# Performance work log

Hardware: AMD Instinct MI355X
Metric: run time of the kernel (lower is better)

The kernel has to match this reference:

```python
import jax, jax.numpy as jnp
import numpy as np

V, H, L, B, S = 32000, 1024, 2, 8, 256


def setup_inputs() -> dict:
    key = jax.random.key(0)
    ks = jax.random.split(key, 12)
    s = 1.0 / np.sqrt(H)  # PyTorch LSTM/Linear init range
    u = lambda k, shape: jax.random.uniform(k, shape, jnp.float32, -s, s)
    return {
        "x": jax.random.randint(ks[0], (B, S), 0, V, dtype=jnp.int32),
        "h0": jnp.zeros((L, B, H), jnp.float32),
        "c0": jnp.zeros((L, B, H), jnp.float32),
        "w_ih0": u(ks[1], (4 * H, V)),
        "w_hh0": u(ks[2], (4 * H, H)),
        "b_ih0": u(ks[3], (4 * H,)),
        "b_hh0": u(ks[4], (4 * H,)),
        "w_ih1": u(ks[5], (4 * H, H)),
        "w_hh1": u(ks[6], (4 * H, H)),
        "b_ih1": u(ks[7], (4 * H,)),
        "b_hh1": u(ks[8], (4 * H,)),
        "fc_w": u(ks[9], (V, H)),
        "fc_b": u(ks[10], (V,)),
    }


def _lstm_layer(xproj, h0, c0, w_hh):
    """xproj: [S,B,4H] input-to-gate projection (biases folded in).
    Gate order i,f,g,o matches PyTorch."""
    def step(carry, xp):
        h, c = carry
        g = xp + h @ w_hh.T  # [B,4H]
        i, f, gg, o = jnp.split(g, 4, axis=-1)
        c = jax.nn.sigmoid(f) * c + jax.nn.sigmoid(i) * jnp.tanh(gg)
        h = jax.nn.sigmoid(o) * jnp.tanh(c)
        return (h, c), h
    (hT, cT), hs = jax.lax.scan(step, (h0, c0), xproj)
    return hs, hT, cT


def reference(x, h0, c0, w_ih0, w_hh0, b_ih0, b_hh0, w_ih1, w_hh1, b_ih1, b_hh1, fc_w, fc_b):
    # F.one_hot(x, V).float() @ w_ih0.T  ==  gather of rows of w_ih0.T (identical math)
    xp0 = jnp.take(w_ih0.T, x, axis=0) + (b_ih0 + b_hh0)  # [B,S,4H]
    xp0 = xp0.transpose(1, 0, 2)  # [S,B,4H] for time-major scan
    h1s, h1T, c1T = _lstm_layer(xp0, h0[0], c0[0], w_hh0)
    xp1 = h1s @ w_ih1.T + (b_ih1 + b_hh1)  # [S,B,4H]
    h2s, h2T, c2T = _lstm_layer(xp1, h0[1], c0[1], w_hh1)
    out = h2s.transpose(1, 0, 2).reshape(-1, H)  # [B*S,H]
    logits = out @ fc_w.T + fc_b  # [B*S,V]
    hn = jnp.stack([h1T, h2T])
    cn = jnp.stack([c1T, c2T])
    return logits, (hn, cn)
```

## Files before the change

### kernel.cpp

```cpp
#include <hip/hip_runtime.h>
#include <cmath>

typedef float  f32x4  __attribute__((ext_vector_type(4)));
typedef float  f32x2  __attribute__((ext_vector_type(2)));
typedef __bf16 bf16x8 __attribute__((ext_vector_type(8)));

static constexpr int HN  = 1024;
static constexpr int VN  = 32000;
static constexpr int BN  = 8;
static constexpr int SN  = 256;
static constexpr int H4N = 4096;

__global__ __launch_bounds__(256) void k_gather(const int* __restrict__ x,
    const float* __restrict__ w_ih0, const float* __restrict__ b_ih0,
    const float* __restrict__ b_hh0, float* __restrict__ xp) {
  int bid = blockIdx.x;
  int t = bid >> 3, b = bid & 7;
  int tok = x[b * SN + t];
  const float* col = w_ih0 + tok;
  float* dst = xp + (size_t)bid * H4N;
  for (int r = threadIdx.x; r < H4N; r += 256)
    dst[r] = col[(size_t)r * VN] + b_ih0[r] + b_hh0[r];
}

__global__ __launch_bounds__(256, 1) void k_lstm(
    const float* __restrict__ xp,
    const float* __restrict__ w_hh,
    const float* __restrict__ h0,
    const float* __restrict__ c0,
    float* __restrict__ hs,
    float* __restrict__ hn, float* __restrict__ cn,
    unsigned* __restrict__ bar) {
  __shared__ float wL[16][1024];
  __shared__ float hL[8192];
  __shared__ float red[8][4][4][32];
  __shared__ float gates[16][8];
  __shared__ float cL[32];

  const int tid = threadIdx.x;
  const int wg  = blockIdx.x;
  const int u0  = wg * 4;

  for (int it = 0; it < 16; ++it) {
    int g = it >> 2, u = it & 3;
    int k4 = tid;
    int k4s = k4 ^ ((k4 >> 3) & 7);
    f32x4 v = *(const f32x4*)&w_hh[((size_t)g * HN + u0 + u) * HN + k4 * 4];
    *(f32x4*)&wL[it][k4s * 4] = v;
  }
  if (tid < 32) cL[tid] = c0[(tid & 7) * HN + u0 + (tid >> 3)];

  const int ks = tid & 31, rg = (tid >> 5) & 3, bg = tid >> 7;
  const int ksx = ks & 7;
  const int hb = tid & 7;
  const int hk = tid >> 3;

  const int prow = tid >> 3, pb = tid & 7;
  const int pg = prow >> 2, pu = prow & 3;
  const size_t pofs = (size_t)pb * H4N + (size_t)pg * HN + u0 + pu;

  for (int t = 0; t < SN; ++t) {
    float xpv = 0.f;
    if (tid < 128) xpv = xp[(size_t)t * (BN * H4N) + pofs];

    const float* hsrc = (t == 0) ? h0 : (hs + (size_t)(t - 1) * (BN * HN));
    const unsigned long long* hsrc8 =
        (const unsigned long long*)hsrc + (size_t)hb * 512 + hk;
    unsigned long long rv[16];
    #pragma unroll
    for (int j = 0; j < 16; ++j)
      rv[j] = __hip_atomic_load((unsigned long long*)(hsrc8 + j * 32),
                                __ATOMIC_RELAXED, __HIP_MEMORY_SCOPE_AGENT);
    #pragma unroll
    for (int j = 0; j < 16; ++j) {
      int k64 = hk + j * 32;
      int k4 = k64 >> 1, half = k64 & 1;
      int idx = ((k4 << 3) | hb) ^ ((k4 >> 3) & 7);
      *(f32x2*)&hL[idx * 4 + half * 2] = __builtin_bit_cast(f32x2, rv[j]);
    }
    __syncthreads();

    float acc[4][4] = {};
    #pragma unroll
    for (int j = 0; j < 8; ++j) {
      int k4 = ks * 8 + j;
      int k4s = k4 ^ ksx;
      f32x4 wv[4], hv[4];
      #pragma unroll
      for (int ri = 0; ri < 4; ++ri)
        wv[ri] = *(const f32x4*)&wL[rg * 4 + ri][k4s * 4];
      #pragma unroll
      for (int bi = 0; bi < 4; ++bi) {
        int idx = ((k4 << 3) | (bg * 4 + bi)) ^ ksx;
        hv[bi] = *(const f32x4*)&hL[idx * 4];
      }
      #pragma unroll
      for (int ri = 0; ri < 4; ++ri)
        #pragma unroll
        for (int bi = 0; bi < 4; ++bi)
          acc[ri][bi] += wv[ri][0]*hv[bi][0] + wv[ri][1]*hv[bi][1]
                       + wv[ri][2]*hv[bi][2] + wv[ri][3]*hv[bi][3];
    }
    #pragma unroll
    for (int ri = 0; ri < 4; ++ri)
      #pragma unroll
      for (int bi = 0; bi < 4; ++bi)
        red[rg * 2 + bg][ri][bi][ks] = acc[ri][bi];
    __syncthreads();

    if (tid < 128) {
      int rrg = prow >> 2, ri = prow & 3, bbg = pb >> 2, bi = pb & 3;
      const float* rp = red[rrg * 2 + bbg][ri][bi];
      float s = 0.f;
      #pragma unroll
      for (int q = 0; q < 32; ++q) s += rp[(q + tid) & 31];
      gates[prow][pb] = s + xpv;
    }
    __syncthreads();

    if (tid < 32) {
      int u = tid >> 3, b = tid & 7;
      float gi = gates[0 * 4 + u][b], gf = gates[1 * 4 + u][b];
      float gg = gates[2 * 4 + u][b], go = gates[3 * 4 + u][b];
      float si = 1.f / (1.f + expf(-gi));
      float sf = 1.f / (1.f + expf(-gf));
      float so = 1.f / (1.f + expf(-go));
      float c = sf * cL[tid] + si * tanhf(gg);
      float h = so * tanhf(c);
      cL[tid] = c;
      __hip_atomic_store(&hs[(size_t)t * (BN * HN) + b * HN + u0 + u], h,
                         __ATOMIC_RELAXED, __HIP_MEMORY_SCOPE_AGENT);
      if (t == SN - 1) {
        hn[b * HN + u0 + u] = h;
        cn[b * HN + u0 + u] = c;
      }
    }

    if (t != SN - 1) {
      if (tid == 0) {
        asm volatile("s_waitcnt vmcnt(0)" ::: "memory");
        __hip_atomic_fetch_add(&bar[(wg & 7) * 32], 1u,
                               __ATOMIC_RELAXED, __HIP_MEMORY_SCOPE_AGENT);
      }
      if (tid < 8) {
        unsigned tgt = 32u * (unsigned)(t + 1);
        while (__hip_atomic_load(&bar[tid * 32], __ATOMIC_RELAXED,
                                 __HIP_MEMORY_SCOPE_AGENT) < tgt)
          __builtin_amdgcn_s_sleep(1);
      }
      __syncthreads();
    } else {
      __syncthreads();
    }
  }
}

__global__ __launch_bounds__(256) void k_split(const float* __restrict__ src,
    __bf16* __restrict__ hi, __bf16* __restrict__ lo) {
  int i = (blockIdx.x * 256 + threadIdx.x) * 4;
  f32x4 v = *(const f32x4*)&src[i];
  #pragma unroll
  for (int j = 0; j < 4; ++j) {
    __bf16 h = (__bf16)v[j];
    hi[i + j] = h;
    lo[i + j] = (__bf16)(v[j] - (float)h);
  }
}

__global__ __launch_bounds__(256) void k_gemm(const __bf16* __restrict__ Ahi,
    const __bf16* __restrict__ Alo, const float* __restrict__ Bsrc,
    const float* __restrict__ bias1, const float* __restrict__ bias2,
    float* __restrict__ C, int Mt, int N, int permute) {
  __shared__ __bf16 sAh[128][32], sAl[128][32], sBh[128][32], sBl[128][32];
  int bid = blockIdx.x;
  int tn = bid / Mt, tm = bid % Mt;
  int tid = threadIdx.x, lane = tid & 63, wid = tid >> 6;
  int wr = wid >> 1, wc = wid & 1;
  f32x4 acc[4][4] = {};
  const size_t K = 1024;

  for (int kk = 0; kk < 1024; kk += 32) {
    __syncthreads();
    #pragma unroll
    for (int it = 0; it < 2; ++it) {
      int c = it * 256 + tid;
      int r = c >> 2, k8 = (c & 3) * 8;
      size_t ga = (size_t)(tm * 128 + r) * K + kk + k8;
      *(bf16x8*)&sAh[r][k8] = *(const bf16x8*)&Ahi[ga];
      *(bf16x8*)&sAl[r][k8] = *(const bf16x8*)&Alo[ga];
      size_t gb = (size_t)(tn * 128 + r) * K + kk + k8;
      f32x4 x0 = *(const f32x4*)&Bsrc[gb];
      f32x4 x1 = *(const f32x4*)&Bsrc[gb + 4];
      bf16x8 bh, bl;
      #pragma unroll
      for (int j = 0; j < 4; ++j) {
        __bf16 h0 = (__bf16)x0[j]; bh[j]     = h0; bl[j]     = (__bf16)(x0[j] - (float)h0);
        __bf16 h1 = (__bf16)x1[j]; bh[4 + j] = h1; bl[4 + j] = (__bf16)(x1[j] - (float)h1);
      }
      *(bf16x8*)&sBh[r][k8] = bh;
      *(bf16x8*)&sBl[r][k8] = bl;
    }
    __syncthreads();

    int kq = (lane >> 4) * 8;
    bf16x8 ah[4], al[4], bh[4], bl[4];
    #pragma unroll
    for (int i = 0; i < 4; ++i) {
      int ra = wr * 64 + i * 16 + (lane & 15);
      ah[i] = *(const bf16x8*)&sAh[ra][kq];
      al[i] = *(const bf16x8*)&sAl[ra][kq];
      int rb = wc * 64 + i * 16 + (lane & 15);
      bh[i] = *(const bf16x8*)&sBh[rb][kq];
      bl[i] = *(const bf16x8*)&sBl[rb][kq];
    }
    #pragma unroll
    for (int i = 0; i < 4; ++i)
      #pragma unroll
      for (int j = 0; j < 4; ++j) {
        acc[i][j] = __builtin_amdgcn_mfma_f32_16x16x32_bf16(ah[i], bh[j], acc[i][j], 0, 0, 0);
        acc[i][j] = __builtin_amdgcn_mfma_f32_16x16x32_bf16(ah[i], bl[j], acc[i][j], 0, 0, 0);
        acc[i][j] = __builtin_amdgcn_mfma_f32_16x16x32_bf16(al[i], bh[j], acc[i][j], 0, 0, 0);
      }
  }

  #pragma unroll
  for (int j = 0; j < 4; ++j) {
    int gcol = tn * 128 + wc * 64 + j * 16 + (lane & 15);
    float bv = bias1[gcol] + (bias2 ? bias2[gcol] : 0.f);
    #pragma unroll
    for (int i = 0; i < 4; ++i) {
      #pragma unroll
      for (int r = 0; r < 4; ++r) {
        int row = tm * 128 + wr * 64 + i * 16 + ((lane >> 4) << 2) + r;
        int orow = permute ? ((row & 7) * 256 + (row >> 3)) : row;
        C[(size_t)orow * N + gcol] = acc[i][j][r] + bv;
      }
    }
  }
}

extern "C" void kernel_launch(void* const* d_in, const int* in_sizes, int n_in,
                              void* d_out, int out_size, void* d_ws, size_t ws_size,
                              hipStream_t stream) {
  (void)in_sizes; (void)n_in; (void)out_size; (void)ws_size;
  const int*   x     = (const int*)  d_in[0];
  const float* h0    = (const float*)d_in[1];
  const float* c0    = (const float*)d_in[2];
  const float* w_ih0 = (const float*)d_in[3];
  const float* w_hh0 = (const float*)d_in[4];
  const float* b_ih0 = (const float*)d_in[5];
  const float* b_hh0 = (const float*)d_in[6];
  const float* w_ih1 = (const float*)d_in[7];
  const float* w_hh1 = (const float*)d_in[8];
  const float* b_ih1 = (const float*)d_in[9];
  const float* b_hh1 = (const float*)d_in[10];
  const float* fc_w  = (const float*)d_in[11];
  const float* fc_b  = (const float*)d_in[12];
  float* out = (float*)d_out;
  float* ws  = (float*)d_ws;

  float* xp   = ws;
  float* h1s  = ws + 8388608;
  float* h2s  = ws + 10485760;
  __bf16* Ahi = (__bf16*)(ws + 12582912);
  __bf16* Alo = (__bf16*)(ws + 13631488);
  unsigned* bar = (unsigned*)(ws + 14680064);

  const size_t LOG = (size_t)2048 * VN;
  float* hn = out + LOG;
  float* cn = out + LOG + 16384;

  hipMemsetAsync(bar, 0, 4096 * sizeof(unsigned), stream);

  k_gather<<<SN * BN, 256, 0, stream>>>(x, w_ih0, b_ih0, b_hh0, xp);

  k_lstm<<<256, 256, 0, stream>>>(xp, w_hh0, h0, c0, h1s, hn, cn, bar);

  k_split<<<2048, 256, 0, stream>>>(h1s, Ahi, Alo);
  k_gemm<<<16 * 32, 256, 0, stream>>>(Ahi, Alo, w_ih1, b_ih1, b_hh1, xp,
                                      16, H4N, 0);

  k_lstm<<<256, 256, 0, stream>>>(xp, w_hh1, h0 + BN * HN, c0 + BN * HN,
                                  h2s, hn + BN * HN, cn + BN * HN, bar + 2048);

  k_split<<<2048, 256, 0, stream>>>(h2s, Ahi, Alo);
  k_gemm<<<16 * 250, 256, 0, stream>>>(Ahi, Alo, fc_w, fc_b, nullptr, out,
                                       16, VN, 1);
}
```

Measured before the change: 4.546 ms.

## Use per-XCD leader blocks to relay hidden state through local buffers

Replaces the all-to-all grid barrier in the persistent LSTM kernel with a hierarchical scheme. One elected leader block per XCD polls the 64 per-group counters, reads the previous hidden state and copies it into a per-XCD double-buffered scratch area, then raises a flag. The other blocks on that XCD wait only on the flag and read the copy with sc0 loads, so that cross-die polling and coherent traffic are confined to one block per XCD. The cost is an extra serialized hop (leader copy, then flag) on the critical path every step, and correctness now depends on how blocks are placed across XCDs and on the memory ordering of the relaxed atomics.

```diff
diff --git a/kernel.cpp b/kernel.cpp
--- a/kernel.cpp
+++ b/kernel.cpp
@@ -30,16 +30,28 @@
     const float* __restrict__ c0,
     float* __restrict__ hs,
     float* __restrict__ hn, float* __restrict__ cn,
-    unsigned* __restrict__ bar) {
+    unsigned* __restrict__ bar,
+    unsigned* __restrict__ flag,
+    unsigned* __restrict__ elect,
+    float* __restrict__ xbuf) {
   __shared__ float wL[16][1024];
   __shared__ float hL[8192];
   __shared__ float red[8][4][4][32];
   __shared__ float gates[16][8];
   __shared__ float cL[32];
+  __shared__ unsigned meta[2];
 
   const int tid = threadIdx.x;
   const int wg  = blockIdx.x;
   const int u0  = wg * 4;
+
+  unsigned xcc;
+  asm volatile("s_getreg_b32 %0, hwreg(HW_REG_XCC_ID)" : "=s"(xcc));
+  if (tid == 0) {
+    meta[0] = xcc & 7;
+    meta[1] = __hip_atomic_fetch_add(&elect[(xcc & 7) * 32], 1u,
+                                     __ATOMIC_RELAXED, __HIP_MEMORY_SCOPE_AGENT);
+  }
 
   for (int it = 0; it < 16; ++it) {
     int g = it >> 2, u = it & 3;
@@ -49,6 +61,9 @@
     *(f32x4*)&wL[it][k4s * 4] = v;
   }
   if (tid < 32) cL[tid] = c0[(tid & 7) * HN + u0 + (tid >> 3)];
+  __syncthreads();
+  const int  myxcd  = (int)meta[0];
+  const bool leader = (meta[1] == 0u);
 
   const int ks = tid & 31, rg = (tid >> 5) & 3, bg = tid >> 7;
   const int ksx = ks & 7;
@@ -63,14 +78,73 @@
     float xpv = 0.f;
     if (tid < 128) xpv = xp[(size_t)t * (BN * H4N) + pofs];
 
-    const float* hsrc = (t == 0) ? h0 : (hs + (size_t)(t - 1) * (BN * HN));
-    const unsigned long long* hsrc8 =
-        (const unsigned long long*)hsrc + (size_t)hb * 512 + hk;
+    float* xbp = xbuf + ((size_t)(t & 1) * 8 + myxcd) * 8192;
     unsigned long long rv[16];
-    #pragma unroll
-    for (int j = 0; j < 16; ++j)
-      rv[j] = __hip_atomic_load((unsigned long long*)(hsrc8 + j * 32),
-                                __ATOMIC_RELAXED, __HIP_MEMORY_SCOPE_AGENT);
+    if (t == 0) {
+      const unsigned long long* s8 =
+          (const unsigned long long*)h0 + (size_t)hb * 512 + hk;
+      #pragma unroll
+      for (int j = 0; j < 16; ++j) rv[j] = s8[j * 32];
+    } else if (leader) {
+      if (tid < 64) {
+        unsigned tgt = 4u * (unsigned)t;
+        while (__hip_atomic_load(&bar[tid * 32], __ATOMIC_RELAXED,
+                                 __HIP_MEMORY_SCOPE_AGENT) < tgt)
+          __builtin_amdgcn_s_sleep(1);
+      }
+      __syncthreads();
+      const unsigned long long* hsrc8 =
+          (const unsigned long long*)(hs + (size_t)(t - 1) * (BN * HN))
+          + (size_t)hb * 512 + hk;
+      #pragma unroll
+      for (int j = 0; j < 16; ++j)
+        rv[j] = __hip_atomic_load((unsigned long long*)(hsrc8 + j * 32),
+                                  __ATOMIC_RELAXED, __HIP_MEMORY_SCOPE_AGENT);
+      unsigned long long* xb8 =
+          (unsigned long long*)xbp + (size_t)hb * 512 + hk;
+      #pragma unroll
+      for (int j = 0; j < 16; ++j) xb8[j * 32] = rv[j];
+    } else {
+      if (tid == 0) {
+        while (__hip_atomic_load(&flag[myxcd * 32], __ATOMIC_RELAXED,
+                                 __HIP_MEMORY_SCOPE_AGENT) < (unsigned)t)
+          __builtin_amdgcn_s_sleep(1);
+      }
+      __syncthreads();
+      const unsigned long long* xb8 =
+          (const unsigned long long*)xbp + (size_t)hb * 512 + hk;
+      unsigned long long a = (unsigned long long)xb8;
+      unsigned long long r0, r1, r2, r3, r4, r5, r6, r7;
+      unsigned long long r8, r9, r10, r11, r12, r13, r14, r15;
+      asm volatile(
+        "global_load_dwordx2 %0, %16, off sc0\n\t"
+        "global_load_dwordx2 %1, %16, off offset:256 sc0\n\t"
+        "global_load_dwordx2 %2, %16, off offset:512 sc0\n\t"
+        "global_load_dwordx2 %3, %16, off offset:768 sc0\n\t"
+        "global_load_dwordx2 %4, %16, off offset:1024 sc0\n\t"
+        "global_load_dwordx2 %5, %16, off offset:1280 sc0\n\t"
+        "global_load_dwordx2 %6, %16, off offset:1536 sc0\n\t"
+        "global_load_dwordx2 %7, %16, off offset:1792 sc0\n\t"
+        "global_load_dwordx2 %8, %16, off offset:2048 sc0\n\t"
+        "global_load_dwordx2 %9, %16, off offset:2304 sc0\n\t"
+        "global_load_dwordx2 %10, %16, off offset:2560 sc0\n\t"
+        "global_load_dwordx2 %11, %16, off offset:2816 sc0\n\t"
+        "global_load_dwordx2 %12, %16, off offset:3072 sc0\n\t"
+        "global_load_dwordx2 %13, %16, off offset:3328 sc0\n\t"
+        "global_load_dwordx2 %14, %16, off offset:3584 sc0\n\t"
+        "global_load_dwordx2 %15, %16, off offset:3840 sc0\n\t"
+        "s_waitcnt vmcnt(0)"
+        : "=&v"(r0), "=&v"(r1), "=&v"(r2), "=&v"(r3),
+          "=&v"(r4), "=&v"(r5), "=&v"(r6), "=&v"(r7),
+          "=&v"(r8), "=&v"(r9), "=&v"(r10), "=&v"(r11),
+          "=&v"(r12), "=&v"(r13), "=&v"(r14), "=&v"(r15)
+        : "v"(a) : "memory");
+      rv[0] = r0;  rv[1] = r1;  rv[2] = r2;  rv[3] = r3;
+      rv[4] = r4;  rv[5] = r5;  rv[6] = r6;  rv[7] = r7;
+      rv[8] = r8;  rv[9] = r9;  rv[10] = r10; rv[11] = r11;
+      rv[12] = r12; rv[13] = r13; rv[14] = r14; rv[15] = r15;
+    }
+
     #pragma unroll
     for (int j = 0; j < 16; ++j) {
       int k64 = hk + j * 32;
@@ -79,6 +153,9 @@
       *(f32x2*)&hL[idx * 4 + half * 2] = __builtin_bit_cast(f32x2, rv[j]);
     }
     __syncthreads();
+    if (t > 0 && leader && tid == 0)
+      __hip_atomic_fetch_add(&flag[myxcd * 32], 1u,
+                             __ATOMIC_RELAXED, __HIP_MEMORY_SCOPE_AGENT);
 
     float acc[4][4] = {};
     #pragma unroll
@@ -139,14 +216,8 @@
     if (t != SN - 1) {
       if (tid == 0) {
         asm volatile("s_waitcnt vmcnt(0)" ::: "memory");
-        __hip_atomic_fetch_add(&bar[(wg & 7) * 32], 1u,
+        __hip_atomic_fetch_add(&bar[(wg >> 2) * 32], 1u,
                                __ATOMIC_RELAXED, __HIP_MEMORY_SCOPE_AGENT);
-      }
-      if (tid < 8) {
-        unsigned tgt = 32u * (unsigned)(t + 1);
-        while (__hip_atomic_load(&bar[tid * 32], __ATOMIC_RELAXED,
-                                 __HIP_MEMORY_SCOPE_AGENT) < tgt)
-          __builtin_amdgcn_s_sleep(1);
       }
       __syncthreads();
     } else {
@@ -264,24 +335,34 @@
   float* h2s  = ws + 10485760;
   __bf16* Ahi = (__bf16*)(ws + 12582912);
   __bf16* Alo = (__bf16*)(ws + 13631488);
-  unsigned* bar = (unsigned*)(ws + 14680064);
+  unsigned* U = (unsigned*)(ws + 14680064);
+  unsigned* bar0   = U;
+  unsigned* bar1   = U + 2048;
+  unsigned* flag0  = U + 4096;
+  unsigned* flag1  = U + 4352;
+  unsigned* elect0 = U + 4608;
+  unsigned* elect1 = U + 4864;
+  float* xbuf0 = ws + 14688256;
+  float* xbuf1 = ws + 14819328;
 
   const size_t LOG = (size_t)2048 * VN;
   float* hn = out + LOG;
   float* cn = out + LOG + 16384;
 
-  hipMemsetAsync(bar, 0, 4096 * sizeof(unsigned), stream);
+  hipMemsetAsync(U, 0, 5120 * sizeof(unsigned), stream);
 
   k_gather<<<SN * BN, 256, 0, stream>>>(x, w_ih0, b_ih0, b_hh0, xp);
 
-  k_lstm<<<256, 256, 0, stream>>>(xp, w_hh0, h0, c0, h1s, hn, cn, bar);
+  k_lstm<<<256, 256, 0, stream>>>(xp, w_hh0, h0, c0, h1s, hn, cn,
+                                  bar0, flag0, elect0, xbuf0);
 
   k_split<<<2048, 256, 0, stream>>>(h1s, Ahi, Alo);
   k_gemm<<<16 * 32, 256, 0, stream>>>(Ahi, Alo, w_ih1, b_ih1, b_hh1, xp,
                                       16, H4N, 0);
 
   k_lstm<<<256, 256, 0, stream>>>(xp, w_hh1, h0 + BN * HN, c0 + BN * HN,
-                                  h2s, hn + BN * HN, cn + BN * HN, bar + 2048);
+                                  h2s, hn + BN * HN, cn + BN * HN,
+                                  bar1, flag1, elect1, xbuf1);
 
   k_split<<<2048, 256, 0, stream>>>(h2s, Ahi, Alo);
   k_gemm<<<16 * 250, 256, 0, stream>>>(Ahi, Alo, fc_w, fc_b, nullptr, out,
```

Result: slower. 5.650 ms (+24.3%).

## Fuse layer-0 embedding gather into LSTM and use per-step flag synchronization

Applied to the files above, without the earlier changes.

Removes the separate gather kernel by having the first-layer LSTM kernel read the token column of w_ih0 plus the bias on the fly each step. The global counter barrier is replaced with per-step, per-workgroup tag stores; every thread polls one workgroup's tag before reading the previous hidden state. This cuts a kernel launch and the intermediate xp write/read, and avoids atomic contention. In exchange, strided weight loads now sit inside the latency-critical recurrence and polling traffic increases.

```diff
diff --git a/kernel.cpp b/kernel.cpp
--- a/kernel.cpp
+++ b/kernel.cpp
@@ -11,31 +11,24 @@
 static constexpr int SN  = 256;
 static constexpr int H4N = 4096;
 
-__global__ __launch_bounds__(256) void k_gather(const int* __restrict__ x,
-    const float* __restrict__ w_ih0, const float* __restrict__ b_ih0,
-    const float* __restrict__ b_hh0, float* __restrict__ xp) {
-  int bid = blockIdx.x;
-  int t = bid >> 3, b = bid & 7;
-  int tok = x[b * SN + t];
-  const float* col = w_ih0 + tok;
-  float* dst = xp + (size_t)bid * H4N;
-  for (int r = threadIdx.x; r < H4N; r += 256)
-    dst[r] = col[(size_t)r * VN] + b_ih0[r] + b_hh0[r];
-}
-
 __global__ __launch_bounds__(256, 1) void k_lstm(
     const float* __restrict__ xp,
+    const float* __restrict__ wtok,
+    const int*   __restrict__ xtok,
+    const float* __restrict__ bi,
+    const float* __restrict__ bh,
     const float* __restrict__ w_hh,
     const float* __restrict__ h0,
     const float* __restrict__ c0,
     float* __restrict__ hs,
     float* __restrict__ hn, float* __restrict__ cn,
-    unsigned* __restrict__ bar) {
+    unsigned* __restrict__ tags) {
   __shared__ float wL[16][1024];
   __shared__ float hL[8192];
   __shared__ float red[8][4][4][32];
   __shared__ float gates[16][8];
   __shared__ float cL[32];
+  __shared__ int   tokL[SN * BN / 2 * 0 + 2048];
 
   const int tid = threadIdx.x;
   const int wg  = blockIdx.x;
@@ -49,6 +42,12 @@
     *(f32x4*)&wL[it][k4s * 4] = v;
   }
   if (tid < 32) cL[tid] = c0[(tid & 7) * HN + u0 + (tid >> 3)];
+  if (xtok) {
+    for (int j = 0; j < 8; ++j) {
+      int idx = j * 256 + tid;
+      tokL[(idx & 255) * 8 + (idx >> 8)] = xtok[idx];
+    }
+  }
 
   const int ks = tid & 31, rg = (tid >> 5) & 3, bg = tid >> 7;
   const int ksx = ks & 7;
@@ -57,20 +56,44 @@
 
   const int prow = tid >> 3, pb = tid & 7;
   const int pg = prow >> 2, pu = prow & 3;
-  const size_t pofs = (size_t)pb * H4N + (size_t)pg * HN + u0 + pu;
+  const int growg = pg * HN + u0 + pu;
+  const size_t pofs = (size_t)pb * H4N + growg;
+  float bsum = 0.f;
+  if (bi && tid < 128) bsum = bi[growg] + bh[growg];
+  __syncthreads();
 
   for (int t = 0; t < SN; ++t) {
     float xpv = 0.f;
-    if (tid < 128) xpv = xp[(size_t)t * (BN * H4N) + pofs];
-
-    const float* hsrc = (t == 0) ? h0 : (hs + (size_t)(t - 1) * (BN * HN));
-    const unsigned long long* hsrc8 =
-        (const unsigned long long*)hsrc + (size_t)hb * 512 + hk;
+    if (tid < 128) {
+      if (wtok) {
+        int tok = tokL[t * 8 + pb];
+        xpv = wtok[(size_t)growg * VN + tok] + bsum;
+      } else {
+        xpv = xp[(size_t)t * (BN * H4N) + pofs];
+      }
+    }
+
     unsigned long long rv[16];
-    #pragma unroll
-    for (int j = 0; j < 16; ++j)
-      rv[j] = __hip_atomic_load((unsigned long long*)(hsrc8 + j * 32),
-                                __ATOMIC_RELAXED, __HIP_MEMORY_SCOPE_AGENT);
+    if (t == 0) {
+      const unsigned long long* s8 =
+          (const unsigned long long*)h0 + (size_t)hb * 512 + hk;
+      #pragma unroll
+      for (int j = 0; j < 16; ++j) rv[j] = s8[j * 32];
+    } else {
+      const unsigned* tg = tags + (size_t)(t - 1) * 256 + tid;
+      while (__hip_atomic_load(tg, __ATOMIC_RELAXED,
+                               __HIP_MEMORY_SCOPE_AGENT) != (unsigned)t)
+        __builtin_amdgcn_s_sleep(1);
+      __syncthreads();
+      const unsigned long long* hsrc8 =
+          (const unsigned long long*)(hs + (size_t)(t - 1) * (BN * HN))
+          + (size_t)hb * 512 + hk;
+      #pragma unroll
+      for (int j = 0; j < 16; ++j)
+        rv[j] = __hip_atomic_load((unsigned long long*)(hsrc8 + j * 32),
+                                  __ATOMIC_RELAXED, __HIP_MEMORY_SCOPE_AGENT);
+    }
+
     #pragma unroll
     for (int j = 0; j < 16; ++j) {
       int k64 = hk + j * 32;
@@ -90,27 +113,27 @@
       for (int ri = 0; ri < 4; ++ri)
         wv[ri] = *(const f32x4*)&wL[rg * 4 + ri][k4s * 4];
       #pragma unroll
-      for (int bi = 0; bi < 4; ++bi) {
-        int idx = ((k4 << 3) | (bg * 4 + bi)) ^ ksx;
-        hv[bi] = *(const f32x4*)&hL[idx * 4];
+      for (int bi2 = 0; bi2 < 4; ++bi2) {
+        int idx = ((k4 << 3) | (bg * 4 + bi2)) ^ ksx;
+        hv[bi2] = *(const f32x4*)&hL[idx * 4];
       }
       #pragma unroll
       for (int ri = 0; ri < 4; ++ri)
         #pragma unroll
-        for (int bi = 0; bi < 4; ++bi)
-          acc[ri][bi] += wv[ri][0]*hv[bi][0] + wv[ri][1]*hv[bi][1]
-                       + wv[ri][2]*hv[bi][2] + wv[ri][3]*hv[bi][3];
+        for (int bi2 = 0; bi2 < 4; ++bi2)
+          acc[ri][bi2] += wv[ri][0]*hv[bi2][0] + wv[ri][1]*hv[bi2][1]
+                        + wv[ri][2]*hv[bi2][2] + wv[ri][3]*hv[bi2][3];
     }
     #pragma unroll
     for (int ri = 0; ri < 4; ++ri)
       #pragma unroll
-      for (int bi = 0; bi < 4; ++bi)
-        red[rg * 2 + bg][ri][bi][ks] = acc[ri][bi];
+      for (int bi2 = 0; bi2 < 4; ++bi2)
+        red[rg * 2 + bg][ri][bi2][ks] = acc[ri][bi2];
     __syncthreads();
 
     if (tid < 128) {
-      int rrg = prow >> 2, ri = prow & 3, bbg = pb >> 2, bi = pb & 3;
-      const float* rp = red[rrg * 2 + bbg][ri][bi];
+      int rrg = prow >> 2, ri = prow & 3, bbg = pb >> 2, bi2 = pb & 3;
+      const float* rp = red[rrg * 2 + bbg][ri][bi2];
       float s = 0.f;
       #pragma unroll
       for (int q = 0; q < 32; ++q) s += rp[(q + tid) & 31];
@@ -135,22 +158,10 @@
         cn[b * HN + u0 + u] = c;
       }
     }
-
-    if (t != SN - 1) {
-      if (tid == 0) {
-        asm volatile("s_waitcnt vmcnt(0)" ::: "memory");
-        __hip_atomic_fetch_add(&bar[(wg & 7) * 32], 1u,
-                               __ATOMIC_RELAXED, __HIP_MEMORY_SCOPE_AGENT);
-      }
-      if (tid < 8) {
-        unsigned tgt = 32u * (unsigned)(t + 1);
-        while (__hip_atomic_load(&bar[tid * 32], __ATOMIC_RELAXED,
-                                 __HIP_MEMORY_SCOPE_AGENT) < tgt)
-          __builtin_amdgcn_s_sleep(1);
-      }
-      __syncthreads();
-    } else {
-      __syncthreads();
+    if (t != SN - 1 && tid == 0) {
+      asm volatile("s_waitcnt vmcnt(0)" ::: "memory");
+      __hip_atomic_store(&tags[(size_t)t * 256 + wg], (unsigned)(t + 1),
+                         __ATOMIC_RELAXED, __HIP_MEMORY_SCOPE_AGENT);
     }
   }
 }
@@ -264,24 +275,24 @@
   float* h2s  = ws + 10485760;
   __bf16* Ahi = (__bf16*)(ws + 12582912);
   __bf16* Alo = (__bf16*)(ws + 13631488);
-  unsigned* bar = (unsigned*)(ws + 14680064);
+  unsigned* tags = (unsigned*)(ws + 14680064);
 
   const size_t LOG = (size_t)2048 * VN;
   float* hn = out + LOG;
   float* cn = out + LOG + 16384;
 
-  hipMemsetAsync(bar, 0, 4096 * sizeof(unsigned), stream);
-
-  k_gather<<<SN * BN, 256, 0, stream>>>(x, w_ih0, b_ih0, b_hh0, xp);
-
-  k_lstm<<<256, 256, 0, stream>>>(xp, w_hh0, h0, c0, h1s, hn, cn, bar);
+  hipMemsetAsync(tags, 0, 65536 * sizeof(unsigned), stream);
+  k_lstm<<<256, 256, 0, stream>>>(nullptr, w_ih0, x, b_ih0, b_hh0,
+                                  w_hh0, h0, c0, h1s, hn, cn, tags);
 
   k_split<<<2048, 256, 0, stream>>>(h1s, Ahi, Alo);
   k_gemm<<<16 * 32, 256, 0, stream>>>(Ahi, Alo, w_ih1, b_ih1, b_hh1, xp,
                                       16, H4N, 0);
 
-  k_lstm<<<256, 256, 0, stream>>>(xp, w_hh1, h0 + BN * HN, c0 + BN * HN,
-                                  h2s, hn + BN * HN, cn + BN * HN, bar + 2048);
+  hipMemsetAsync(tags, 0, 65536 * sizeof(unsigned), stream);
+  k_lstm<<<256, 256, 0, stream>>>(xp, nullptr, nullptr, nullptr, nullptr,
+                                  w_hh1, h0 + BN * HN, c0 + BN * HN,
+                                  h2s, hn + BN * HN, cn + BN * HN, tags);
 
   k_split<<<2048, 256, 0, stream>>>(h2s, Ahi, Alo);
   k_gemm<<<16 * 250, 256, 0, stream>>>(Ahi, Alo, fc_w, fc_b, nullptr, out,
```

Result: slower. 5.105 ms (+12.3%).
